# Kernel tuning notes

Measured on AMD Instinct MI355X. Metric: run time of the kernel, lower is better.

## Reference

```python
import jax, jax.numpy as jnp
import numpy as np

B, C, H, W, L = 8, 512, 32, 32, 10
CQK = C // 8
EPS = 1e-5


def conv1x1(x, Wt, b):
    # 1x1 conv == per-pixel linear: [O,C] x [B,C,H,W] -> [B,O,H,W]
    return jnp.einsum('oc,bchw->bohw', Wt, x) + b[None, :, None, None]


def batchnorm_train(x, g, b):
    # BatchNorm2d in training mode: batch stats over (N,H,W), biased variance
    m = x.mean(axis=(0, 2, 3))
    v = x.var(axis=(0, 2, 3))
    inv = jax.lax.rsqrt(v + EPS)
    return (x - m[None, :, None, None]) * (g * inv)[None, :, None, None] + b[None, :, None, None]


def setup_inputs() -> dict:
    key = jax.random.key(0)
    ks = jax.random.split(key, 24)
    s = lambda n: 1.0 / np.sqrt(n)
    inp = {
        'x': jax.random.normal(ks[0], (B, C, H, W), jnp.float32),
        'y': jax.random.normal(ks[1], (B, C, H, W), jnp.float32),
        'x_hidden': jax.random.normal(ks[2], (L, B, C, H, W), jnp.float32),
        'y_hidden': jax.random.normal(ks[3], (L, B, C, H, W), jnp.float32),
        'qW': jax.random.normal(ks[4], (CQK, C), jnp.float32) * s(C),
        'qb': jnp.zeros((CQK,), jnp.float32),
        'kW': jax.random.normal(ks[5], (CQK, C), jnp.float32) * s(C),
        'kb': jnp.zeros((CQK,), jnp.float32),
        'v1W': jax.random.normal(ks[6], (C, C), jnp.float32) * s(C),
        'v1b': jnp.zeros((C,), jnp.float32),
        'v2W': jax.random.normal(ks[7], (C, C), jnp.float32) * s(C),
        'v2b': jnp.zeros((C,), jnp.float32),
        'hw1': jnp.ones((L,), jnp.float32),
        'hw2': jnp.ones((L,), jnp.float32),
        'g1W1': jax.random.normal(ks[8], (64, C), jnp.float32) * s(C),
        'g1b1': jnp.zeros((64,), jnp.float32),
        'g1W2': jax.random.normal(ks[9], (1, 64), jnp.float32) * s(64),
        'g1b2': jnp.zeros((1,), jnp.float32),
        'g2W1': jax.random.normal(ks[10], (64, C), jnp.float32) * s(C),
        'g2b1': jnp.zeros((64,), jnp.float32),
        'g2W2': jax.random.normal(ks[11], (1, 64), jnp.float32) * s(64),
        'g2b2': jnp.zeros((1,), jnp.float32),
        'rW1': jax.random.normal(ks[12], (C, C), jnp.float32) * s(C),
        'rb1': jnp.zeros((C,), jnp.float32),
        'bn1g': jnp.ones((C,), jnp.float32),
        'bn1b': jnp.zeros((C,), jnp.float32),
        'rW2': jax.random.normal(ks[13], (C, C), jnp.float32) * s(C),
        'rb2': jnp.zeros((C,), jnp.float32),
        'bn2g': jnp.ones((C,), jnp.float32),
        'bn2b': jnp.zeros((C,), jnp.float32),
    }
    return inp


def reference(x, y, x_hidden, y_hidden, qW, qb, kW, kb, v1W, v1b, v2W, v2b,
              hw1, hw2, g1W1, g1b1, g1W2, g1b2, g2W1, g2b1, g2W2, g2b2,
              rW1, rb1, bn1g, bn1b, rW2, rb2, bn2g, bn2b):
    b_, c_, h_, w_ = x.shape
    n = h_ * w_

    def residual(z):
        z1 = jax.nn.relu(batchnorm_train(conv1x1(z, rW1, rb1), bn1g, bn1b))
        return batchnorm_train(conv1x1(z1, rW2, rb2), bn2g, bn2b)

    # QKV projections (1x1 convs), flattened to tokens
    q = conv1x1(x, qW, qb).reshape(b_, CQK, n).transpose(0, 2, 1)   # [B,N,Cqk]
    k = conv1x1(y, kW, kb).reshape(b_, CQK, n)                       # [B,Cqk,N]
    v1 = conv1x1(x, v1W, v1b).reshape(b_, c_, n)                     # [B,C,N]
    v2 = conv1x1(y, v2W, v2b).reshape(b_, c_, n)

    attn = jax.nn.softmax(jnp.einsum('bnd,bdm->bnm', q, k), axis=-1)  # [B,N,N]
    out1 = jnp.einsum('bcn,bmn->bcm', v1, attn).reshape(b_, c_, h_, w_)  # v1 @ attn^T
    out2 = jnp.einsum('bcn,bnm->bcm', v2, attn).reshape(b_, c_, h_, w_)  # v2 @ attn

    # hidden-layer weighted channel means -> gamma scalars
    num_layers = min(x_hidden.shape[0], L)
    xw = jax.nn.softmax(hw1[:num_layers])
    yw = jax.nn.softmax(hw2[:num_layers])
    x_hw = jnp.einsum('l,lbc->bc', xw, x_hidden[:num_layers].mean(axis=(3, 4)))  # [B,C]
    y_hw = jnp.einsum('l,lbc->bc', yw, y_hidden[:num_layers].mean(axis=(3, 4)))

    def gamma_gen(v, W1, b1, W2, b2):
        h1 = jax.nn.relu(v @ W1.T + b1)
        return (h1 @ W2.T + b2).reshape(b_, 1, 1, 1)

    gamma1 = gamma_gen(x_hw, g1W1, g1b1, g1W2, g1b2)
    gamma2 = gamma_gen(y_hw, g2W1, g2b1, g2W2, g2b2)

    out1 = jax.nn.relu(residual(gamma1 * out1) + x)
    out2 = jax.nn.relu(residual(gamma2 * out2) + y)
    return out1, out2
```

## Files before the change

kernel.cpp:

```cpp
#include <hip/hip_runtime.h>

#define BB 8
#define CC 512
#define NT 1024
#define LL 10
#define DQK 64
#define BN_EPS 1e-5f

using u16 = unsigned short;
typedef __attribute__((ext_vector_type(8))) short short8;
typedef __attribute__((ext_vector_type(4))) float f32x4;
typedef __attribute__((ext_vector_type(4))) float nf4;

__device__ __forceinline__ float waveSum(float v) {
#pragma unroll
  for (int o = 32; o; o >>= 1) v += __shfl_down(v, o, 64);
  return v;
}
__device__ __forceinline__ float waveMax(float v) {
#pragma unroll
  for (int o = 32; o; o >>= 1) v = fmaxf(v, __shfl_down(v, o, 64));
  return v;
}
__device__ __forceinline__ u16 f2bf(float f) {
  unsigned u = __float_as_uint(f);
  u += 0x7FFFu + ((u >> 16) & 1u);
  return (u16)(u >> 16);
}
__device__ __forceinline__ float bf2f(u16 h) {
  return __uint_as_float(((unsigned)h) << 16);
}
__device__ __forceinline__ void g2l16(const u16* g, void* l) {
  __builtin_amdgcn_global_load_lds(
      (const __attribute__((address_space(1))) unsigned int*)g,
      (__attribute__((address_space(3))) unsigned int*)l, 16, 0, 0);
}

struct PreArgs {
  const float *xh, *yh;
  float* lm;
  const float *v1W, *v2W, *rW1, *rW2;
  u16* Wdst;
  const float *qW, *kW;
  u16 *qh, *ql, *kh, *kl;
  const float *qb, *kb, *v1b, *v2b;
  float *qkb, *vb;
  const float *x, *y;
  u16 *xth, *xtl, *yth, *ytl;
};
__global__ __launch_bounds__(256) void pre_kernel(PreArgs a) {
  __shared__ float t[64][65];
  const int blk = blockIdx.x;
  if (blk < 20480) {
    int wid = blk * 4 + (threadIdx.x >> 6);
    int lane = threadIdx.x & 63;
    const int LBC = LL * BB * CC;
    const float* src = a.xh;
    int r = wid;
    if (wid >= LBC) { src = a.yh; r = wid - LBC; }
    const nf4* p = (const nf4*)(src + (size_t)r * NT);
    nf4 v0 = __builtin_nontemporal_load(p + lane);
    nf4 v1 = __builtin_nontemporal_load(p + 64 + lane);
    nf4 v2 = __builtin_nontemporal_load(p + 128 + lane);
    nf4 v3 = __builtin_nontemporal_load(p + 192 + lane);
    float s = ((v0.x + v0.y) + (v0.z + v0.w)) + ((v1.x + v1.y) + (v1.z + v1.w)) +
              ((v2.x + v2.y) + (v2.z + v2.w)) + ((v3.x + v3.y) + (v3.z + v3.w));
    s = waveSum(s);
    if (lane == 0) a.lm[wid] = s * (1.0f / NT);
  } else if (blk < 21504) {
    int rel = blk - 20480;
    const float* srcs[4] = {a.v1W, a.v2W, a.rW1, a.rW2};
    const float4* s4 = (const float4*)srcs[rel >> 8];
    int r = rel & 255;
    float4 v = s4[(size_t)r * 256 + threadIdx.x];
    uint2 o;
    o.x = (unsigned)f2bf(v.x) | ((unsigned)f2bf(v.y) << 16);
    o.y = (unsigned)f2bf(v.z) | ((unsigned)f2bf(v.w) << 16);
    ((uint2*)a.Wdst)[(size_t)rel * 256 + threadIdx.x] = o;
  } else if (blk < 21568) {
    int rel = blk - 21504;
    if (rel == 0) {
      int tt = threadIdx.x;
      if (tt < 64) a.qkb[tt] = a.qb[tt];
      else if (tt < 128) a.qkb[tt] = a.kb[tt - 64];
      a.vb[tt] = a.v1b[tt]; a.vb[tt + 256] = a.v1b[tt + 256];
      a.vb[tt + 512] = a.v2b[tt]; a.vb[tt + 768] = a.v2b[tt + 256];
    }
    const float* src = (rel < 32) ? a.qW : a.kW;
    u16* dh = (rel < 32) ? a.qh : a.kh;
    u16* dl = (rel < 32) ? a.ql : a.kl;
    int r = rel & 31;
    float4 v = ((const float4*)src)[(size_t)r * 256 + threadIdx.x];
    u16 h0 = f2bf(v.x), h1 = f2bf(v.y), h2 = f2bf(v.z), h3 = f2bf(v.w);
    u16 l0 = f2bf(v.x - bf2f(h0)), l1 = f2bf(v.y - bf2f(h1));
    u16 l2 = f2bf(v.z - bf2f(h2)), l3 = f2bf(v.w - bf2f(h3));
    uint2 oh, ol;
    oh.x = (unsigned)h0 | ((unsigned)h1 << 16); oh.y = (unsigned)h2 | ((unsigned)h3 << 16);
    ol.x = (unsigned)l0 | ((unsigned)l1 << 16); ol.y = (unsigned)l2 | ((unsigned)l3 << 16);
    ((uint2*)dh)[(size_t)r * 256 + threadIdx.x] = oh;
    ((uint2*)dl)[(size_t)r * 256 + threadIdx.x] = ol;
  } else {
    int rel = blk - 21568;
    int z = rel >> 7;
    const float* src = (z < 8) ? a.x : a.y;
    u16* dh = (z < 8) ? a.xth : a.yth;
    u16* dl = (z < 8) ? a.xtl : a.ytl;
    int b = z & 7;
    int n0 = (rel & 15) * 64, c0 = ((rel >> 4) & 7) * 64;
    int tc = threadIdx.x & 63, tr = threadIdx.x >> 6;
    const float* S = src + ((size_t)b * CC + c0) * NT + n0;
#pragma unroll
    for (int r = 0; r < 16; r++) {
      int c = tr + r * 4;
      t[c][tc] = S[(size_t)c * NT + tc];
    }
    __syncthreads();
    size_t base = ((size_t)b * NT + n0) * CC + c0;
#pragma unroll
    for (int r = 0; r < 16; r++) {
      int n = tr + r * 4;
      float v = t[tc][n];
      u16 h = f2bf(v);
      dh[base + (size_t)n * CC + tc] = h;
      dl[base + (size_t)n * CC + tc] = f2bf(v - bf2f(h));
    }
  }
}

__global__ __launch_bounds__(256) void gamma_kernel(
    const float* __restrict__ lm,
    const float* __restrict__ hw1, const float* __restrict__ hw2,
    const float* __restrict__ g1W1, const float* __restrict__ g1b1,
    const float* __restrict__ g1W2, const float* __restrict__ g1b2,
    const float* __restrict__ g2W1, const float* __restrict__ g2b1,
    const float* __restrict__ g2W2, const float* __restrict__ g2b2,
    float* __restrict__ gamma) {
  int which = blockIdx.x >> 3;
  int b = blockIdx.x & 7;
  const float* hw = which ? hw2 : hw1;
  const float* W1 = which ? g2W1 : g1W1;
  const float* b1 = which ? g2b1 : g1b1;
  const float* W2 = which ? g2W2 : g1W2;
  const float* b2 = which ? g2b2 : g1b2;
  __shared__ float sxhw[CC];
  __shared__ float wsm[LL];
  if (threadIdx.x == 0) {
    float mx = -1e30f;
    for (int l = 0; l < LL; l++) mx = fmaxf(mx, hw[l]);
    float den = 0.f, e[LL];
    for (int l = 0; l < LL; l++) { e[l] = __expf(hw[l] - mx); den += e[l]; }
    for (int l = 0; l < LL; l++) wsm[l] = e[l] / den;
  }
  __syncthreads();
  const float* lmb = lm + (size_t)which * LL * BB * CC + b * CC;
  for (int c = threadIdx.x; c < CC; c += blockDim.x) {
    float a = 0.f;
    for (int l = 0; l < LL; l++) a += wsm[l] * lmb[l * BB * CC + c];
    sxhw[c] = a;
  }
  __syncthreads();
  float contrib = 0.f;
  if (threadIdx.x < 64) {
    int d = threadIdx.x;
    float a = b1[d];
    const float* wr = W1 + d * CC;
    for (int c = 0; c < CC; c++) a = fmaf(wr[c], sxhw[c], a);
    contrib = W2[d] * fmaxf(a, 0.f);
  }
  contrib = waveSum(contrib);
  if (threadIdx.x == 0) gamma[which * BB + b] = contrib + b2[0];
}

__global__ __launch_bounds__(256) void transpose_attn_kernel(
    const u16* __restrict__ attn, u16* __restrict__ attnT) {
  __shared__ u16 t[64][66];
  int b = blockIdx.z;
  int n0 = blockIdx.y * 64, m0 = blockIdx.x * 64;
  int tc = threadIdx.x & 63, tr = threadIdx.x >> 6;
  const u16* S = attn + ((size_t)b * NT + n0) * NT + m0;
#pragma unroll
  for (int r = 0; r < 16; r++) {
    int nr = tr + r * 4;
    t[nr][tc] = S[(size_t)nr * NT + tc];
  }
  __syncthreads();
  u16* D = attnT + ((size_t)b * NT + m0) * NT + n0;
#pragma unroll
  for (int r = 0; r < 16; r++) {
    int mr = tr + r * 4;
    D[(size_t)mr * NT + tc] = t[tc][mr];
  }
}

template <int BN>
__global__ __launch_bounds__(256) void gemm_bf16(
    const u16* __restrict__ A, long long sA, int lda,
    const u16* __restrict__ B, long long sB, long long sB2, int ldb,
    void* __restrict__ C, long long sC, int ldc,
    int K, int storef32,
    const float* __restrict__ bias_row, int brs,
    const float* __restrict__ scale) {
  constexpr int BM = 128, BK = 32;
  constexpr int WN = (BN == 128) ? 2 : 1;
  constexpr int WM = 4 / WN;
  constexpr int FM = BM / (WM * 16);
  constexpr int FN = BN / (WN * 16);
  __shared__ u16 As[BM * BK];
  __shared__ u16 Bs[BN * BK];
  const int bz = blockIdx.z;
  const int i0 = blockIdx.y * BM;
  const int j0 = blockIdx.x * BN;
  const u16* Ab = A + (size_t)bz * sA + (size_t)i0 * lda;
  const u16* Bb = B + (size_t)(bz & 7) * sB + (size_t)(bz >> 3) * sB2 + (size_t)j0 * ldb;
  const int tid = threadIdx.x;
  const int lane = tid & 63;
  const int wave = tid >> 6;
  const int wr = wave / WN, wc = wave % WN;
  const int fr = lane & 15;
  const int kg = lane >> 4;
  const int arow = tid >> 2;
  const int aq = tid & 3;

  f32x4 acc[FM][FN] = {};

  for (int k0 = 0; k0 < K; k0 += BK) {
#pragma unroll
    for (int c = 0; c < (BM * BK * 2) / 4096; c++)
      g2l16(Ab + (size_t)(arow + c * 64) * lda + k0 + aq * 8,
            (char*)As + c * 4096 + tid * 16);
#pragma unroll
    for (int c = 0; c < (BN * BK * 2) / 4096; c++)
      g2l16(Bb + (size_t)(arow + c * 64) * ldb + k0 + aq * 8,
            (char*)Bs + c * 4096 + tid * 16);
    __syncthreads();
    short8 fa[FM], fb[FN];
#pragma unroll
    for (int i = 0; i < FM; i++)
      fa[i] = *(const short8*)&As[(wr * FM * 16 + i * 16 + fr) * BK + kg * 8];
#pragma unroll
    for (int j = 0; j < FN; j++)
      fb[j] = *(const short8*)&Bs[(wc * FN * 16 + j * 16 + fr) * BK + kg * 8];
#pragma unroll
    for (int i = 0; i < FM; i++)
#pragma unroll
      for (int j = 0; j < FN; j++)
        acc[i][j] = __builtin_amdgcn_mfma_f32_16x16x32_bf16(fa[i], fb[j], acc[i][j], 0, 0, 0);
    __syncthreads();
  }

  const float scl = scale ? scale[bz] : 1.0f;
  const float* brow = bias_row ? bias_row + (size_t)bz * brs : nullptr;
  float* Cf = (float*)C + (size_t)bz * sC;
  u16* Ch = (u16*)C + (size_t)bz * sC;
#pragma unroll
  for (int i = 0; i < FM; i++) {
#pragma unroll
    for (int j = 0; j < FN; j++) {
      int col = j0 + wc * FN * 16 + j * 16 + fr;
#pragma unroll
      for (int r = 0; r < 4; r++) {
        int row = i0 + wr * FM * 16 + i * 16 + kg * 4 + r;
        float rb = brow ? brow[row] : 0.0f;
        float v = (acc[i][j][r] + rb) * scl;
        if (storef32) Cf[(size_t)row * ldc + col] = v;
        else Ch[(size_t)row * ldc + col] = f2bf(v);
      }
    }
  }
}

__global__ __launch_bounds__(256) void gemm_split(
    const u16* __restrict__ Ah_, const u16* __restrict__ Al_, long long sA, int lda,
    const u16* __restrict__ Bh_, const u16* __restrict__ Bl_, long long sB, int ldb,
    float* __restrict__ Cf, u16* __restrict__ Ch, u16* __restrict__ Cl,
    long long sC, int ldc, int K, const float* __restrict__ bias_col, int bcs) {
  constexpr int BM = 128, BN = 64, BK = 32;
  constexpr int FM = 2, FN = 4;
  __shared__ u16 Ahs[BM * BK];
  __shared__ u16 Als[BM * BK];
  __shared__ u16 Bhs[BN * BK];
  __shared__ u16 Bls[BN * BK];
  const int bz = blockIdx.z;
  const int i0 = blockIdx.y * BM;
  const int j0 = blockIdx.x * BN;
  const u16* Abh = Ah_ + (size_t)bz * sA + (size_t)i0 * lda;
  const u16* Abl = Al_ + (size_t)bz * sA + (size_t)i0 * lda;
  const u16* Bbh = Bh_ + (size_t)bz * sB + (size_t)j0 * ldb;
  const u16* Bbl = Bl_ + (size_t)bz * sB + (size_t)j0 * ldb;
  const int tid = threadIdx.x;
  const int lane = tid & 63;
  const int wr = tid >> 6;
  const int fr = lane & 15;
  const int kg = lane >> 4;
  const int arow = tid >> 2;
  const int aq = tid & 3;

  f32x4 acc[FM][FN] = {};

  for (int k0 = 0; k0 < K; k0 += BK) {
#pragma unroll
    for (int c = 0; c < 2; c++) {
      g2l16(Abh + (size_t)(arow + c * 64) * lda + k0 + aq * 8,
            (char*)Ahs + c * 4096 + tid * 16);
      g2l16(Abl + (size_t)(arow + c * 64) * lda + k0 + aq * 8,
            (char*)Als + c * 4096 + tid * 16);
    }
    g2l16(Bbh + (size_t)arow * ldb + k0 + aq * 8, (char*)Bhs + tid * 16);
    g2l16(Bbl + (size_t)arow * ldb + k0 + aq * 8, (char*)Bls + tid * 16);
    __syncthreads();
    short8 fah[FM], fal[FM], fbh[FN], fbl[FN];
#pragma unroll
    for (int i = 0; i < FM; i++) {
      fah[i] = *(const short8*)&Ahs[(wr * 32 + i * 16 + fr) * BK + kg * 8];
      fal[i] = *(const short8*)&Als[(wr * 32 + i * 16 + fr) * BK + kg * 8];
    }
#pragma unroll
    for (int j = 0; j < FN; j++) {
      fbh[j] = *(const short8*)&Bhs[(j * 16 + fr) * BK + kg * 8];
      fbl[j] = *(const short8*)&Bls[(j * 16 + fr) * BK + kg * 8];
    }
#pragma unroll
    for (int i = 0; i < FM; i++)
#pragma unroll
      for (int j = 0; j < FN; j++) {
        acc[i][j] = __builtin_amdgcn_mfma_f32_16x16x32_bf16(fah[i], fbh[j], acc[i][j], 0, 0, 0);
        acc[i][j] = __builtin_amdgcn_mfma_f32_16x16x32_bf16(fah[i], fbl[j], acc[i][j], 0, 0, 0);
        acc[i][j] = __builtin_amdgcn_mfma_f32_16x16x32_bf16(fal[i], fbh[j], acc[i][j], 0, 0, 0);
      }
    __syncthreads();
  }

  const float* bcol = bias_col ? bias_col + (size_t)bz * bcs : nullptr;
  float* Cfb = Cf ? Cf + (size_t)bz * sC : nullptr;
  u16* Chb = Ch ? Ch + (size_t)bz * sC : nullptr;
  u16* Clb = Cl ? Cl + (size_t)bz * sC : nullptr;
#pragma unroll
  for (int i = 0; i < FM; i++) {
#pragma unroll
    for (int j = 0; j < FN; j++) {
      int col = j0 + j * 16 + fr;
      float cb = bcol ? bcol[col] : 0.0f;
#pragma unroll
      for (int r = 0; r < 4; r++) {
        int row = i0 + wr * 32 + i * 16 + kg * 4 + r;
        float v = acc[i][j][r] + cb;
        if (Cfb) {
          Cfb[(size_t)row * ldc + col] = v;
        } else {
          u16 h = f2bf(v);
          Chb[(size_t)row * ldc + col] = h;
          Clb[(size_t)row * ldc + col] = f2bf(v - bf2f(h));
        }
      }
    }
  }
}

__global__ __launch_bounds__(256) void softmax_bf_kernel(
    const float* __restrict__ S, u16* __restrict__ A) {
  const float4* row = (const float4*)(S + (size_t)blockIdx.x * NT);
  float4 v = row[threadIdx.x];
  __shared__ float sb[4];
  __shared__ float broad;
  int lane = threadIdx.x & 63, wid = threadIdx.x >> 6;
  float mx = fmaxf(fmaxf(v.x, v.y), fmaxf(v.z, v.w));
  mx = waveMax(mx);
  if (lane == 0) sb[wid] = mx;
  __syncthreads();
  if (threadIdx.x == 0) broad = fmaxf(fmaxf(sb[0], sb[1]), fmaxf(sb[2], sb[3]));
  __syncthreads();
  mx = broad;
  v.x = __expf(v.x - mx); v.y = __expf(v.y - mx);
  v.z = __expf(v.z - mx); v.w = __expf(v.w - mx);
  float s = v.x + v.y + v.z + v.w;
  s = waveSum(s);
  __syncthreads();
  if (lane == 0) sb[wid] = s;
  __syncthreads();
  if (threadIdx.x == 0) broad = sb[0] + sb[1] + sb[2] + sb[3];
  __syncthreads();
  float inv = 1.0f / broad;
  uint2 o;
  o.x = (unsigned)f2bf(v.x * inv) | ((unsigned)f2bf(v.y * inv) << 16);
  o.y = (unsigned)f2bf(v.z * inv) | ((unsigned)f2bf(v.w * inv) << 16);
  ((uint2*)(A + (size_t)blockIdx.x * NT))[threadIdx.x] = o;
}

__global__ __launch_bounds__(256) void bnstats_tm_part(
    const u16* __restrict__ Z, float* __restrict__ pS, float* __restrict__ pS2) {
  int blk = blockIdx.x;
  int chain = blk >> 8, bl = blk & 255;
  int c2 = threadIdx.x;
  float s0 = 0, s1 = 0, q0 = 0, q1 = 0;
  const u16* base = Z + (size_t)blk * 32 * CC;
#pragma unroll 4
  for (int r = 0; r < 32; r++) {
    unsigned u = *(const unsigned*)(base + (size_t)r * CC + c2 * 2);
    float a = bf2f((u16)u), b = bf2f((u16)(u >> 16));
    s0 += a; q0 += a * a; s1 += b; q1 += b * b;
  }
  size_t co = (size_t)chain * 512;
  pS[(co + c2 * 2) * 256 + bl] = s0;
  pS[(co + c2 * 2 + 1) * 256 + bl] = s1;
  pS2[(co + c2 * 2) * 256 + bl] = q0;
  pS2[(co + c2 * 2 + 1) * 256 + bl] = q1;
}
__global__ __launch_bounds__(256) void bnstats_tm_reduce(
    const float* __restrict__ pS, const float* __restrict__ pS2,
    const float* __restrict__ g, const float* __restrict__ bet,
    float* __restrict__ scale, float* __restrict__ shift) {
  int cg = blockIdx.x;
  int c = cg & 511;
  float s = pS[(size_t)cg * 256 + threadIdx.x];
  float s2 = pS2[(size_t)cg * 256 + threadIdx.x];
  s = waveSum(s); s2 = waveSum(s2);
  __shared__ float sb[8];
  int lane = threadIdx.x & 63, wid = threadIdx.x >> 6;
  if (lane == 0) { sb[wid] = s; sb[wid + 4] = s2; }
  __syncthreads();
  if (threadIdx.x == 0) {
    float S = sb[0] + sb[1] + sb[2] + sb[3];
    float S2 = sb[4] + sb[5] + sb[6] + sb[7];
    const float invn = 1.0f / (BB * NT);
    float mean = S * invn;
    float var = S2 * invn - mean * mean;
    float inv = rsqrtf(var + BN_EPS);
    float sc = g[c] * inv;
    scale[cg] = sc;
    shift[cg] = bet[c] - mean * sc;
  }
}

__global__ __launch_bounds__(256) void bnstats_cm(
    const u16* __restrict__ Z, const float* __restrict__ g, const float* __restrict__ bet,
    float* __restrict__ scale, float* __restrict__ shift) {
  int cg = blockIdx.x;
  int c = cg & 511;
  const uint2* row = (const uint2*)(Z + (size_t)cg * (BB * NT));
  float s = 0, s2 = 0;
#pragma unroll
  for (int it = 0; it < 8; it++) {
    uint2 u = row[threadIdx.x + it * 256];
    float a = bf2f((u16)u.x), b = bf2f((u16)(u.x >> 16));
    float d = bf2f((u16)u.y), e = bf2f((u16)(u.y >> 16));
    s += a + b + d + e;
    s2 += a * a + b * b + d * d + e * e;
  }
  s = waveSum(s); s2 = waveSum(s2);
  __shared__ float sb[8];
  int lane = threadIdx.x & 63, wid = threadIdx.x >> 6;
  if (lane == 0) { sb[wid] = s; sb[wid + 4] = s2; }
  __syncthreads();
  if (threadIdx.x == 0) {
    float S = sb[0] + sb[1] + sb[2] + sb[3];
    float S2 = sb[4] + sb[5] + sb[6] + sb[7];
    const float invn = 1.0f / (BB * NT);
    float mean = S * invn;
    float var = S2 * invn - mean * mean;
    float inv = rsqrtf(var + BN_EPS);
    float sc = g[c] * inv;
    scale[cg] = sc;
    shift[cg] = bet[c] - mean * sc;
  }
}

__global__ __launch_bounds__(256) void bn_apply_kernel(
    const u16* __restrict__ Z, u16* __restrict__ Zo,
    const float* __restrict__ scale, const float* __restrict__ shift) {
  size_t e4 = (size_t)blockIdx.x * 256 + threadIdx.x;
  int chain = (int)(e4 >> 20);
  int c = (int)(e4 & 127) * 4 + chain * 512;
  uint2 u = ((const uint2*)Z)[e4];
  float a = bf2f((u16)u.x), b = bf2f((u16)(u.x >> 16));
  float d = bf2f((u16)u.y), e = bf2f((u16)(u.y >> 16));
  a = fmaxf(fmaf(a, scale[c], shift[c]), 0.f);
  b = fmaxf(fmaf(b, scale[c + 1], shift[c + 1]), 0.f);
  d = fmaxf(fmaf(d, scale[c + 2], shift[c + 2]), 0.f);
  e = fmaxf(fmaf(e, scale[c + 3], shift[c + 3]), 0.f);
  uint2 o;
  o.x = (unsigned)f2bf(a) | ((unsigned)f2bf(b) << 16);
  o.y = (unsigned)f2bf(d) | ((unsigned)f2bf(e) << 16);
  ((uint2*)Zo)[e4] = o;
}

__global__ __launch_bounds__(256) void bn_final_kernel(
    const u16* __restrict__ Z2, const float* __restrict__ X, const float* __restrict__ Y,
    const float* __restrict__ scale, const float* __restrict__ shift,
    float* __restrict__ Out) {
  size_t e = (size_t)blockIdx.x * 256 + threadIdx.x;
  int chain = (int)(e >> 20);
  size_t ec = e & 1048575;
  int c = (int)(ec >> 11);
  int r = (int)(ec & 2047);
  int b = r >> 8;
  uint2 u = ((const uint2*)Z2)[e];
  float a0 = bf2f((u16)u.x), a1 = bf2f((u16)(u.x >> 16));
  float a2 = bf2f((u16)u.y), a3 = bf2f((u16)(u.y >> 16));
  float sc = scale[c + chain * 512], sh = shift[c + chain * 512];
  size_t xi = ((size_t)b * CC + c) * 256 + (r & 255);
  const float* Xs = chain ? Y : X;
  float4 xv = ((const float4*)Xs)[xi];
  float4 o;
  o.x = fmaxf(fmaf(a0, sc, sh) + xv.x, 0.f);
  o.y = fmaxf(fmaf(a1, sc, sh) + xv.y, 0.f);
  o.z = fmaxf(fmaf(a2, sc, sh) + xv.z, 0.f);
  o.w = fmaxf(fmaf(a3, sc, sh) + xv.w, 0.f);
  ((float4*)(Out + (size_t)chain * 4194304))[xi] = o;
}

extern "C" void kernel_launch(void* const* d_in, const int* in_sizes, int n_in,
                              void* d_out, int out_size, void* d_ws, size_t ws_size,
                              hipStream_t stream) {
  (void)in_sizes; (void)n_in; (void)out_size; (void)ws_size;
  const float* x    = (const float*)d_in[0];
  const float* y    = (const float*)d_in[1];
  const float* xh   = (const float*)d_in[2];
  const float* yh   = (const float*)d_in[3];
  const float* qW   = (const float*)d_in[4];
  const float* qb   = (const float*)d_in[5];
  const float* kW   = (const float*)d_in[6];
  const float* kb   = (const float*)d_in[7];
  const float* v1W  = (const float*)d_in[8];
  const float* v1b  = (const float*)d_in[9];
  const float* v2W  = (const float*)d_in[10];
  const float* v2b  = (const float*)d_in[11];
  const float* hw1  = (const float*)d_in[12];
  const float* hw2  = (const float*)d_in[13];
  const float* g1W1 = (const float*)d_in[14];
  const float* g1b1 = (const float*)d_in[15];
  const float* g1W2 = (const float*)d_in[16];
  const float* g1b2 = (const float*)d_in[17];
  const float* g2W1 = (const float*)d_in[18];
  const float* g2b1 = (const float*)d_in[19];
  const float* g2W2 = (const float*)d_in[20];
  const float* g2b2 = (const float*)d_in[21];
  const float* rW1  = (const float*)d_in[22];
  const float* bn1g = (const float*)d_in[24];
  const float* bn1b = (const float*)d_in[25];
  const float* rW2  = (const float*)d_in[26];
  const float* bn2g = (const float*)d_in[28];
  const float* bn2b = (const float*)d_in[29];
  float* out = (float*)d_out;

  float* ws  = (float*)d_ws;
  float* lm  = ws;
  float* gam = ws + 81920;
  float* scA = ws + 81936;
  float* shA = ws + 82960;
  float* qkb = ws + 83984;
  float* vb  = ws + 84112;
  float* pS  = ws + 85136;
  float* pS2 = ws + 347280;
  float* S   = ws + 609424;
  u16* U     = (u16*)(ws + 8998032);
  u16* Wqh = U;
  u16* Wql = U + 32768;
  u16* Wkh = U + 65536;
  u16* Wkl = U + 98304;
  u16* Wv1 = U + 131072;
  u16* Wv2 = U + 393216;
  u16* Wr1 = U + 655360;
  u16* Wr2 = U + 917504;
  u16* xth = U + 1179648;
  u16* yth = xth + 4194304;
  u16* xtl = yth + 4194304;
  u16* ytl = xtl + 4194304;
  u16* q_h = ytl + 4194304;
  u16* q_l = q_h + 524288;
  u16* k_h = q_l + 524288;
  u16* k_l = k_h + 524288;
  u16* v1  = k_l + 524288;
  u16* v2  = v1 + 4194304;
  u16* attn  = v2 + 4194304;
  u16* attnT = attn + 8388608;
  u16* o1t = xth;
  u16* z0  = v1;
  u16* z1  = xth;
  u16* z2  = attn;

  PreArgs pa;
  pa.xh = xh; pa.yh = yh; pa.lm = lm;
  pa.v1W = v1W; pa.v2W = v2W; pa.rW1 = rW1; pa.rW2 = rW2; pa.Wdst = Wv1;
  pa.qW = qW; pa.kW = kW; pa.qh = Wqh; pa.ql = Wql; pa.kh = Wkh; pa.kl = Wkl;
  pa.qb = qb; pa.kb = kb; pa.v1b = v1b; pa.v2b = v2b; pa.qkb = qkb; pa.vb = vb;
  pa.x = x; pa.y = y; pa.xth = xth; pa.xtl = xtl; pa.yth = yth; pa.ytl = ytl;
  pre_kernel<<<23616, 256, 0, stream>>>(pa);
  gamma_kernel<<<16, 256, 0, stream>>>(lm, hw1, hw2, g1W1, g1b1, g1W2, g1b2,
                                       g2W1, g2b1, g2W2, g2b2, gam);

  gemm_bf16<128><<<dim3(64, 4, 2), 256, 0, stream>>>(
      Wv1, 262144, CC, xth, 4194304, 0, CC, v1, 4194304, BB * NT, CC, 0, vb, 512, nullptr);
  gemm_split<<<dim3(1, 64, 2), 256, 0, stream>>>(
      xth, xtl, 4194304, CC, Wqh, Wql, 65536, CC,
      nullptr, q_h, q_l, 1048576, DQK, CC, qkb, 64);

  gemm_split<<<dim3(16, 8, 8), 256, 0, stream>>>(
      q_h, q_l, (long long)NT * DQK, DQK, k_h, k_l, (long long)NT * DQK, DQK,
      S, nullptr, nullptr, (long long)NT * NT, NT, DQK, nullptr, 0);
  softmax_bf_kernel<<<BB * NT, 256, 0, stream>>>(S, attn);
  transpose_attn_kernel<<<dim3(16, 16, 8), 256, 0, stream>>>(attn, attnT);

  gemm_bf16<128><<<dim3(4, 8, 16), 256, 0, stream>>>(
      attn, (long long)NT * NT, NT, v1, NT, 4194304, BB * NT,
      o1t, (long long)NT * CC, CC, NT, 0, nullptr, 0, gam);

  gemm_bf16<128><<<dim3(4, 64, 2), 256, 0, stream>>>(
      o1t, 4194304, CC, Wr1, 0, 0, CC, z0, 4194304, CC, CC, 0, nullptr, 0, nullptr);
  bnstats_tm_part<<<512, 256, 0, stream>>>(z0, pS, pS2);
  bnstats_tm_reduce<<<1024, 256, 0, stream>>>(pS, pS2, bn1g, bn1b, scA, shA);
  bn_apply_kernel<<<8192, 256, 0, stream>>>(z0, z1, scA, shA);
  gemm_bf16<128><<<dim3(64, 4, 2), 256, 0, stream>>>(
      Wr2, 0, CC, z1, 4194304, 0, CC, z2, 4194304, BB * NT, CC, 0, nullptr, 0, nullptr);
  bnstats_cm<<<1024, 256, 0, stream>>>(z2, bn2g, bn2b, scA, shA);
  bn_final_kernel<<<8192, 256, 0, stream>>>(z2, x, y, scA, shA, out);
}
```

Measured before the change: 275.4 us.

## Fuse BatchNorm statistics into GEMM epilogues and use narrower GEMM tiles

The GEMM epilogue now accumulates per-column or per-row sums and sums of squares of its output, as partial sums per block. This replaces the separate stats kernels that reread the bf16 activations from memory, leaving only a small reduction kernel. All GEMM launches also switch from BN=128 to BN=64 tiles, which doubles the grid size for more parallelism. Statistics are now taken from the fp32 values before bf16 rounding, and the extra epilogue work adds register pressure.

```diff
diff --git a/kernel.cpp b/kernel.cpp
--- a/kernel.cpp
+++ b/kernel.cpp
@@ -192,14 +192,15 @@
   }
 }
 
-template <int BN>
+template <int BN, int SMODE>
 __global__ __launch_bounds__(256) void gemm_bf16(
     const u16* __restrict__ A, long long sA, int lda,
     const u16* __restrict__ B, long long sB, long long sB2, int ldb,
     void* __restrict__ C, long long sC, int ldc,
     int K, int storef32,
     const float* __restrict__ bias_row, int brs,
-    const float* __restrict__ scale) {
+    const float* __restrict__ scale,
+    float* __restrict__ pS, float* __restrict__ pS2) {
   constexpr int BM = 128, BK = 32;
   constexpr int WN = (BN == 128) ? 2 : 1;
   constexpr int WM = 4 / WN;
@@ -252,6 +253,8 @@
   const float* brow = bias_row ? bias_row + (size_t)bz * brs : nullptr;
   float* Cf = (float*)C + (size_t)bz * sC;
   u16* Ch = (u16*)C + (size_t)bz * sC;
+  float cs[FN] = {}, cs2[FN] = {};
+  float rs[FM * 4] = {}, rs2[FM * 4] = {};
 #pragma unroll
   for (int i = 0; i < FM; i++) {
 #pragma unroll
@@ -262,10 +265,50 @@
         int row = i0 + wr * FM * 16 + i * 16 + kg * 4 + r;
         float rb = brow ? brow[row] : 0.0f;
         float v = (acc[i][j][r] + rb) * scl;
+        if constexpr (SMODE == 1) { cs[j] += v; cs2[j] += v * v; }
+        if constexpr (SMODE == 2) { rs[i * 4 + r] += v; rs2[i * 4 + r] += v * v; }
         if (storef32) Cf[(size_t)row * ldc + col] = v;
         else Ch[(size_t)row * ldc + col] = f2bf(v);
       }
     }
+  }
+
+  if constexpr (SMODE == 1) {
+    __shared__ float sred[2][4][FN][16];
+#pragma unroll
+    for (int j = 0; j < FN; j++) {
+      float s = cs[j], s2 = cs2[j];
+      s += __shfl_xor(s, 16, 64); s += __shfl_xor(s, 32, 64);
+      s2 += __shfl_xor(s2, 16, 64); s2 += __shfl_xor(s2, 32, 64);
+      if (lane < 16) { sred[0][wr][j][lane] = s; sred[1][wr][j][lane] = s2; }
+    }
+    __syncthreads();
+    if (tid < FN * 16) {
+      int j = tid >> 4, f = tid & 15;
+      float s = sred[0][0][j][f] + sred[0][1][j][f] + sred[0][2][j][f] + sred[0][3][j][f];
+      float s2 = sred[1][0][j][f] + sred[1][1][j][f] + sred[1][2][j][f] + sred[1][3][j][f];
+      int col = j0 + j * 16 + f;
+      int chain = (int)(blockIdx.y >> 6), ib = (int)(blockIdx.y & 63);
+      pS[((size_t)chain * 512 + col) * 64 + ib] = s;
+      pS2[((size_t)chain * 512 + col) * 64 + ib] = s2;
+    }
+  }
+  if constexpr (SMODE == 2) {
+#pragma unroll
+    for (int i = 0; i < FM; i++)
+#pragma unroll
+      for (int r = 0; r < 4; r++) {
+        float s = rs[i * 4 + r], s2 = rs2[i * 4 + r];
+        s += __shfl_xor(s, 1, 64); s += __shfl_xor(s, 2, 64);
+        s += __shfl_xor(s, 4, 64); s += __shfl_xor(s, 8, 64);
+        s2 += __shfl_xor(s2, 1, 64); s2 += __shfl_xor(s2, 2, 64);
+        s2 += __shfl_xor(s2, 4, 64); s2 += __shfl_xor(s2, 8, 64);
+        if (fr == 0) {
+          int row = i0 + wr * FM * 16 + i * 16 + kg * 4 + r;
+          pS[((size_t)bz * 512 + row) * 128 + blockIdx.x] = s;
+          pS2[((size_t)bz * 512 + row) * 128 + blockIdx.x] = s2;
+        }
+      }
   }
 }
 
@@ -386,74 +429,24 @@
   ((uint2*)(A + (size_t)blockIdx.x * NT))[threadIdx.x] = o;
 }
 
-__global__ __launch_bounds__(256) void bnstats_tm_part(
-    const u16* __restrict__ Z, float* __restrict__ pS, float* __restrict__ pS2) {
-  int blk = blockIdx.x;
-  int chain = blk >> 8, bl = blk & 255;
-  int c2 = threadIdx.x;
-  float s0 = 0, s1 = 0, q0 = 0, q1 = 0;
-  const u16* base = Z + (size_t)blk * 32 * CC;
-#pragma unroll 4
-  for (int r = 0; r < 32; r++) {
-    unsigned u = *(const unsigned*)(base + (size_t)r * CC + c2 * 2);
-    float a = bf2f((u16)u), b = bf2f((u16)(u >> 16));
-    s0 += a; q0 += a * a; s1 += b; q1 += b * b;
-  }
-  size_t co = (size_t)chain * 512;
-  pS[(co + c2 * 2) * 256 + bl] = s0;
-  pS[(co + c2 * 2 + 1) * 256 + bl] = s1;
-  pS2[(co + c2 * 2) * 256 + bl] = q0;
-  pS2[(co + c2 * 2 + 1) * 256 + bl] = q1;
-}
-__global__ __launch_bounds__(256) void bnstats_tm_reduce(
+template <int NP>
+__global__ __launch_bounds__(128) void bnstats_reduce_np(
     const float* __restrict__ pS, const float* __restrict__ pS2,
     const float* __restrict__ g, const float* __restrict__ bet,
     float* __restrict__ scale, float* __restrict__ shift) {
   int cg = blockIdx.x;
   int c = cg & 511;
-  float s = pS[(size_t)cg * 256 + threadIdx.x];
-  float s2 = pS2[(size_t)cg * 256 + threadIdx.x];
+  int t = threadIdx.x;
+  float s = 0.f, s2 = 0.f;
+  if (t < NP) { s = pS[(size_t)cg * NP + t]; s2 = pS2[(size_t)cg * NP + t]; }
   s = waveSum(s); s2 = waveSum(s2);
-  __shared__ float sb[8];
-  int lane = threadIdx.x & 63, wid = threadIdx.x >> 6;
-  if (lane == 0) { sb[wid] = s; sb[wid + 4] = s2; }
-  __syncthreads();
-  if (threadIdx.x == 0) {
-    float S = sb[0] + sb[1] + sb[2] + sb[3];
-    float S2 = sb[4] + sb[5] + sb[6] + sb[7];
-    const float invn = 1.0f / (BB * NT);
-    float mean = S * invn;
-    float var = S2 * invn - mean * mean;
-    float inv = rsqrtf(var + BN_EPS);
-    float sc = g[c] * inv;
-    scale[cg] = sc;
-    shift[cg] = bet[c] - mean * sc;
-  }
-}
-
-__global__ __launch_bounds__(256) void bnstats_cm(
-    const u16* __restrict__ Z, const float* __restrict__ g, const float* __restrict__ bet,
-    float* __restrict__ scale, float* __restrict__ shift) {
-  int cg = blockIdx.x;
-  int c = cg & 511;
-  const uint2* row = (const uint2*)(Z + (size_t)cg * (BB * NT));
-  float s = 0, s2 = 0;
-#pragma unroll
-  for (int it = 0; it < 8; it++) {
-    uint2 u = row[threadIdx.x + it * 256];
-    float a = bf2f((u16)u.x), b = bf2f((u16)(u.x >> 16));
-    float d = bf2f((u16)u.y), e = bf2f((u16)(u.y >> 16));
-    s += a + b + d + e;
-    s2 += a * a + b * b + d * d + e * e;
-  }
-  s = waveSum(s); s2 = waveSum(s2);
-  __shared__ float sb[8];
-  int lane = threadIdx.x & 63, wid = threadIdx.x >> 6;
-  if (lane == 0) { sb[wid] = s; sb[wid + 4] = s2; }
-  __syncthreads();
-  if (threadIdx.x == 0) {
-    float S = sb[0] + sb[1] + sb[2] + sb[3];
-    float S2 = sb[4] + sb[5] + sb[6] + sb[7];
+  __shared__ float sb[4];
+  int lane = t & 63, wid = t >> 6;
+  if (lane == 0) { sb[wid] = s; sb[wid + 2] = s2; }
+  __syncthreads();
+  if (t == 0) {
+    float S = sb[0] + sb[1];
+    float S2 = sb[2] + sb[3];
     const float invn = 1.0f / (BB * NT);
     float mean = S * invn;
     float var = S2 * invn - mean * mean;
@@ -588,8 +581,9 @@
   gamma_kernel<<<16, 256, 0, stream>>>(lm, hw1, hw2, g1W1, g1b1, g1W2, g1b2,
                                        g2W1, g2b1, g2W2, g2b2, gam);
 
-  gemm_bf16<128><<<dim3(64, 4, 2), 256, 0, stream>>>(
-      Wv1, 262144, CC, xth, 4194304, 0, CC, v1, 4194304, BB * NT, CC, 0, vb, 512, nullptr);
+  gemm_bf16<64, 0><<<dim3(128, 4, 2), 256, 0, stream>>>(
+      Wv1, 262144, CC, xth, 4194304, 0, CC, v1, 4194304, BB * NT, CC, 0, vb, 512,
+      nullptr, nullptr, nullptr);
   gemm_split<<<dim3(1, 64, 2), 256, 0, stream>>>(
       xth, xtl, 4194304, CC, Wqh, Wql, 65536, CC,
       nullptr, q_h, q_l, 1048576, DQK, CC, qkb, 64);
@@ -600,17 +594,17 @@
   softmax_bf_kernel<<<BB * NT, 256, 0, stream>>>(S, attn);
   transpose_attn_kernel<<<dim3(16, 16, 8), 256, 0, stream>>>(attn, attnT);
 
-  gemm_bf16<128><<<dim3(4, 8, 16), 256, 0, stream>>>(
+  gemm_bf16<64, 0><<<dim3(8, 8, 16), 256, 0, stream>>>(
       attn, (long long)NT * NT, NT, v1, NT, 4194304, BB * NT,
-      o1t, (long long)NT * CC, CC, NT, 0, nullptr, 0, gam);
-
-  gemm_bf16<128><<<dim3(4, 64, 2), 256, 0, stream>>>(
-      o1t, 4194304, CC, Wr1, 0, 0, CC, z0, 4194304, CC, CC, 0, nullptr, 0, nullptr);
-  bnstats_tm_part<<<512, 256, 0, stream>>>(z0, pS, pS2);
-  bnstats_tm_reduce<<<1024, 256, 0, stream>>>(pS, pS2, bn1g, bn1b, scA, shA);
+      o1t, (long long)NT * CC, CC, NT, 0, nullptr, 0, gam, nullptr, nullptr);
+
+  gemm_bf16<64, 1><<<dim3(8, 128, 1), 256, 0, stream>>>(
+      o1t, 0, CC, Wr1, 0, 0, CC, z0, 0, CC, CC, 0, nullptr, 0, nullptr, pS, pS2);
+  bnstats_reduce_np<64><<<1024, 128, 0, stream>>>(pS, pS2, bn1g, bn1b, scA, shA);
   bn_apply_kernel<<<8192, 256, 0, stream>>>(z0, z1, scA, shA);
-  gemm_bf16<128><<<dim3(64, 4, 2), 256, 0, stream>>>(
-      Wr2, 0, CC, z1, 4194304, 0, CC, z2, 4194304, BB * NT, CC, 0, nullptr, 0, nullptr);
-  bnstats_cm<<<1024, 256, 0, stream>>>(z2, bn2g, bn2b, scA, shA);
+  gemm_bf16<64, 2><<<dim3(128, 4, 2), 256, 0, stream>>>(
+      Wr2, 0, CC, z1, 4194304, 0, CC, z2, 4194304, BB * NT, CC, 0, nullptr, 0, nullptr,
+      pS, pS2);
+  bnstats_reduce_np<128><<<1024, 128, 0, stream>>>(pS, pS2, bn2g, bn2b, scA, shA);
   bn_final_kernel<<<8192, 256, 0, stream>>>(z2, x, y, scA, shA, out);
 }
```

After: 278.9 us. No clear change (+1.3%).
